# Performance work log

Hardware: AMD Instinct MI355X
Metric: run time of the kernel (lower is better)

## Reference

```python
import jax, jax.numpy as jnp
import numpy as np

GROUP_SIZE = 128
HIDDEN = 2048
INTER = 5632
TOKENS = 8192
_SHIFTS = jnp.arange(8, dtype=jnp.uint32) * 4  # 4-bit nibbles, 8 per int32


def _pack_rows(nib):
    # nib: [in, out] int values in [0,16); pack 8 consecutive rows into one int32
    r, c = nib.shape
    n = nib.reshape(r // 8, 8, c).astype(jnp.uint32)
    packed = jnp.sum(n << _SHIFTS[None, :, None], axis=1, dtype=jnp.uint32)
    return jax.lax.bitcast_convert_type(packed, jnp.int32)  # [in//8, out]


def _pack_cols(nib):
    # nib: [groups, out]; pack 8 consecutive cols into one int32
    g, o = nib.shape
    n = nib.reshape(g, o // 8, 8).astype(jnp.uint32)
    packed = jnp.sum(n << _SHIFTS[None, None, :], axis=-1, dtype=jnp.uint32)
    return jax.lax.bitcast_convert_type(packed, jnp.int32)  # [groups, out//8]


def _dequant(qweight, qzeros, scales, group_size=GROUP_SIZE):
    # GPTQ int4 dequant: w = (q - (z + 1)) * scale, per group of `group_size` input rows
    in_packed, out = qweight.shape
    in_dim = in_packed * 8
    groups = scales.shape[0]
    sh = jnp.arange(8, dtype=jnp.int32) * 4
    q = (qweight[:, None, :] >> sh[None, :, None]) & 0xF       # [in//8, 8, out]
    q = q.reshape(in_dim, out)
    z = (qzeros[:, :, None] >> sh[None, None, :]) & 0xF        # [groups, out//8, 8]
    z = z.reshape(groups, out)
    gidx = jnp.arange(in_dim) // group_size                    # [in]
    w = (q - (z[gidx] + 1)).astype(scales.dtype) * scales[gidx]
    return w  # [in, out]


def setup_inputs() -> dict:
    key = jax.random.key(0)
    ks = jax.random.split(key, 10)
    x = jax.random.normal(ks[0], (TOKENS, HIDDEN), dtype=jnp.float32)

    def make(kq, kz, ksc, in_dim, out_dim):
        qn = jax.random.randint(kq, (in_dim, out_dim), 0, 16, dtype=jnp.int32)
        zn = jax.random.randint(kz, (in_dim // GROUP_SIZE, out_dim), 0, 16, dtype=jnp.int32)
        sc = jax.random.uniform(ksc, (in_dim // GROUP_SIZE, out_dim), jnp.float32, 1e-3, 2e-2)
        return _pack_rows(qn), _pack_cols(zn), sc

    gq, gz, gs = make(ks[1], ks[2], ks[3], HIDDEN, INTER)
    uq, uz, us = make(ks[4], ks[5], ks[6], HIDDEN, INTER)
    dq, dz, ds = make(ks[7], ks[8], ks[9], INTER, HIDDEN)
    return {
        "x": x,
        "gate_qweight": gq, "gate_qzeros": gz, "gate_scales": gs,
        "up_qweight": uq, "up_qzeros": uz, "up_scales": us,
        "down_qweight": dq, "down_qzeros": dz, "down_scales": ds,
    }


def reference(x, gate_qweight, gate_qzeros, gate_scales,
              up_qweight, up_qzeros, up_scales,
              down_qweight, down_qzeros, down_scales):
    wg = _dequant(gate_qweight, gate_qzeros, gate_scales)  # [H, I]
    wu = _dequant(up_qweight, up_qzeros, up_scales)        # [H, I]
    wd = _dequant(down_qweight, down_qzeros, down_scales)  # [I, H]
    # fused_gate_up: silu(x @ Wg) * (x @ Wu)
    h = jax.nn.silu(x @ wg) * (x @ wu)                     # [T, I]
    return h @ wd                                          # [T, H]
```

## Files before the change

### kernel.cpp

```cpp
#include <hip/hip_runtime.h>
#include <stdint.h>

#define TOKENS 8192
#define HIDDEN 2048
#define INTER  5632

typedef _Float16 f16x8 __attribute__((ext_vector_type(8)));
typedef _Float16 f16x2 __attribute__((ext_vector_type(2)));
typedef float    f32x4 __attribute__((ext_vector_type(4)));
typedef unsigned int uint;

__device__ __forceinline__ void async_copy16(const void* g, void* l) {
  __builtin_amdgcn_global_load_lds(
      (const __attribute__((address_space(1))) uint*)g,
      (__attribute__((address_space(3))) uint*)l, 16, 0, 0);
}

union U8 { uint u[4]; f16x8 v; };
__device__ __forceinline__ f16x8 dq8(uint w, uint sd, uint zd) {
  const f16x2 s = __builtin_bit_cast(f16x2, sd);
  const f16x2 z = __builtin_bit_cast(f16x2, zd);
  U8 r;
  uint t0 = (w & 0x000F000Fu) | 0x64006400u;
  uint t1 = ((w >> 4) & 0x000F000Fu) | 0x64006400u;
  uint t2 = ((w >> 8) & 0x000F000Fu) | 0x64006400u;
  uint t3 = ((w >> 12) & 0x000F000Fu) | 0x64006400u;
  r.u[0] = __builtin_bit_cast(uint, (f16x2)((__builtin_bit_cast(f16x2, t0) - z) * s));
  r.u[1] = __builtin_bit_cast(uint, (f16x2)((__builtin_bit_cast(f16x2, t1) - z) * s));
  r.u[2] = __builtin_bit_cast(uint, (f16x2)((__builtin_bit_cast(f16x2, t2) - z) * s));
  r.u[3] = __builtin_bit_cast(uint, (f16x2)((__builtin_bit_cast(f16x2, t3) - z) * s));
  return r.v;
}

__device__ __forceinline__ uint dupf16(float x) {
  _Float16 h = (_Float16)x;
  unsigned short b = __builtin_bit_cast(unsigned short, h);
  return (uint)b * 0x00010001u;
}

__global__ void k_convert_x(const float* __restrict__ x, _Float16* __restrict__ xs) {
  const int kb = blockIdx.x;
  const int mt = blockIdx.y;
  const int m  = threadIdx.x;
  const float* src = x + (size_t)(mt * 128 + m) * HIDDEN + kb * 8;
  float4 f0 = *(const float4*)src;
  float4 f1 = *(const float4*)(src + 4);
  f16x8 v;
  v[0] = (_Float16)f0.x; v[1] = (_Float16)f1.x;
  v[2] = (_Float16)f0.y; v[3] = (_Float16)f1.y;
  v[4] = (_Float16)f0.z; v[5] = (_Float16)f1.z;
  v[6] = (_Float16)f0.w; v[7] = (_Float16)f1.w;
  *(f16x8*)(xs + ((size_t)(mt * 256 + kb) * 128 + m) * 8) = v;
}

__global__ void k_prep_szgu(const uint* __restrict__ gz, const float* __restrict__ gs,
                            const uint* __restrict__ uz, const float* __restrict__ us,
                            uint4* __restrict__ out) {
  const int n = blockIdx.x * 256 + threadIdx.x;
  const int g = blockIdx.y;
  const int sh = (n & 7) * 4;
  int zg = (int)((gz[(size_t)g * (INTER / 8) + (n >> 3)] >> sh) & 0xFu);
  int zu = (int)((uz[(size_t)g * (INTER / 8) + (n >> 3)] >> sh) & 0xFu);
  float sg = gs[(size_t)g * INTER + n];
  float su = us[(size_t)g * INTER + n];
  out[(size_t)g * INTER + n] =
      make_uint4(dupf16(sg), dupf16((float)(1025 + zg)),
                 dupf16(su), dupf16((float)(1025 + zu)));
}

__global__ void k_prep_szd(const uint* __restrict__ dz, const float* __restrict__ ds,
                           uint2* __restrict__ out) {
  const int n = blockIdx.x * 256 + threadIdx.x;
  const int g = blockIdx.y;
  const int sh = (n & 7) * 4;
  int z = (int)((dz[(size_t)g * (HIDDEN / 8) + (n >> 3)] >> sh) & 0xFu);
  float s = ds[(size_t)g * HIDDEN + n];
  out[(size_t)g * HIDDEN + n] = make_uint2(dupf16(s), dupf16((float)(1025 + z)));
}

__global__ __launch_bounds__(256, 2)
void k_gemm_gateup(const _Float16* __restrict__ xs,
                   const uint* __restrict__ gq,
                   const uint* __restrict__ uq,
                   const uint4* __restrict__ szgu,
                   _Float16* __restrict__ hs) {
  __shared__ char smem[16384 + 4096 + 4096 + 2048];
  _Float16* Al = (_Float16*)smem;
  char* Bgl = smem + 16384;
  char* Bul = smem + 20480;
  char* szl = smem + 24576;

  const int nt = blockIdx.x, mt = blockIdx.y;
  const int tid = threadIdx.x;
  const int wave = tid >> 6, lane = tid & 63;
  const int wm = wave >> 1, wn = wave & 1;
  const int row16 = lane >> 4, col = lane & 15;
  const int slot = wave * 4;

  const _Float16* gA = xs + (size_t)mt * 256 * 1024;

  const int brow = 2 * wave + (lane >> 5);
  const int bcolw = ((lane & 31) * 4) ^ ((brow & 1) << 4);
  const size_t bbase = (size_t)brow * INTER + nt * 128 + bcolw;

  int afo[4];
#pragma unroll
  for (int i = 0; i < 4; ++i)
    afo[i] = (row16 * 128 + wm * 64 + i * 16 + col) * 8;
  int bco[4];
  const int bswz = (row16 & 1) << 4;
#pragma unroll
  for (int ni = 0; ni < 4; ++ni)
    bco[ni] = (wn * 64 + ni * 16 + col) ^ bswz;

  const f32x4 zero = {0.f, 0.f, 0.f, 0.f};
  f32x4 accg[4][4], accu[4][4];
#pragma unroll
  for (int i = 0; i < 4; ++i)
#pragma unroll
    for (int j = 0; j < 4; ++j) { accg[i][j] = zero; accu[i][j] = zero; }

  uint2 szg[4], szu[4];

  for (int kit = 0; kit < HIDDEN / 64; ++kit) {
    __syncthreads();
#pragma unroll
    for (int q = 0; q < 4; ++q) {
      const int c2 = (slot + q) * 64 + lane;
      async_copy16(gA + (size_t)kit * 8192 + (size_t)c2 * 8,
                   (char*)Al + (slot + q) * 1024);
    }
    {
      const size_t go = (size_t)kit * 8 * INTER + bbase;
      async_copy16(gq + go, Bgl + wave * 1024);
      async_copy16(uq + go, Bul + wave * 1024);
    }
    if (((kit & 1) == 0) && wave < 2) {
      const int n = wave * 64 + lane;
      async_copy16(szgu + (size_t)(kit >> 1) * INTER + nt * 128 + n,
                   szl + wave * 1024);
    }
    __syncthreads();
    if ((kit & 1) == 0) {
#pragma unroll
      for (int ni = 0; ni < 4; ++ni) {
        const int n16 = (wn * 64 + ni * 16 + col) * 16;
        szg[ni] = *(const uint2*)(szl + n16);
        szu[ni] = *(const uint2*)(szl + n16 + 8);
      }
    }
#pragma unroll
    for (int ks = 0; ks < 2; ++ks) {
      const int kadd = ks * 4096;
      f16x8 af[4];
#pragma unroll
      for (int i = 0; i < 4; ++i)
        af[i] = *(const f16x8*)(Al + kadd + afo[i]);
      const int bks = (ks * 4 + row16) * 512;
      uint bgw[4], buw[4];
#pragma unroll
      for (int ni = 0; ni < 4; ++ni) {
        bgw[ni] = *(const uint*)(Bgl + bks + bco[ni] * 4);
        buw[ni] = *(const uint*)(Bul + bks + bco[ni] * 4);
      }
      f16x8 bgf[4], buf_[4];
#pragma unroll
      for (int ni = 0; ni < 4; ++ni) {
        bgf[ni] = dq8(bgw[ni], szg[ni].x, szg[ni].y);
        buf_[ni] = dq8(buw[ni], szu[ni].x, szu[ni].y);
      }
#pragma unroll
      for (int mi = 0; mi < 4; ++mi)
#pragma unroll
        for (int ni = 0; ni < 4; ++ni) {
          accg[mi][ni] = __builtin_amdgcn_mfma_f32_16x16x32_f16(af[mi], bgf[ni], accg[mi][ni], 0, 0, 0);
          accu[mi][ni] = __builtin_amdgcn_mfma_f32_16x16x32_f16(af[mi], buf_[ni], accu[mi][ni], 0, 0, 0);
        }
    }
  }
#pragma unroll
  for (int mi = 0; mi < 4; ++mi)
#pragma unroll
    for (int ni = 0; ni < 4; ++ni) {
      const int kg = nt * 128 + wn * 64 + ni * 16 + col;
      const int sub = kg & 7;
      const int pslot = ((sub & 3) << 1) | (sub >> 2);
      const size_t base = (size_t)(mt * (INTER / 8) + (kg >> 3)) * 1024 + pslot;
#pragma unroll
      for (int r = 0; r < 4; ++r) {
        float g = accg[mi][ni][r], u = accu[mi][ni][r];
        float h = g / (1.f + __expf(-g)) * u;
        const int ml = wm * 64 + mi * 16 + row16 * 4 + r;
        hs[base + (size_t)ml * 8] = (_Float16)h;
      }
    }
}

__global__ __launch_bounds__(256, 2)
void k_gemm_down(const _Float16* __restrict__ hs,
                 const uint* __restrict__ dq,
                 const uint2* __restrict__ szd,
                 float* __restrict__ out) {
  __shared__ char smem[16384 + 4096 + 1024];
  _Float16* Al = (_Float16*)smem;
  char* Bl  = smem + 16384;
  char* szl = smem + 20480;

  const int nt = blockIdx.x, mt = blockIdx.y;
  const int tid = threadIdx.x;
  const int wave = tid >> 6, lane = tid & 63;
  const int wm = wave >> 1, wn = wave & 1;
  const int row16 = lane >> 4, col = lane & 15;
  const int slot = wave * 4;

  const _Float16* gA = hs + (size_t)mt * (INTER / 8) * 1024;

  const int brow = 2 * wave + (lane >> 5);
  const int bcolw = ((lane & 31) * 4) ^ ((brow & 1) << 4);
  const size_t bbase = (size_t)brow * HIDDEN + nt * 128 + bcolw;

  int afo[4];
#pragma unroll
  for (int i = 0; i < 4; ++i)
    afo[i] = (row16 * 128 + wm * 64 + i * 16 + col) * 8;
  int bco[4];
  const int bswz = (row16 & 1) << 4;
#pragma unroll
  for (int ni = 0; ni < 4; ++ni)
    bco[ni] = (wn * 64 + ni * 16 + col) ^ bswz;

  const f32x4 zero = {0.f, 0.f, 0.f, 0.f};
  f32x4 acc[4][4];
#pragma unroll
  for (int i = 0; i < 4; ++i)
#pragma unroll
    for (int j = 0; j < 4; ++j) acc[i][j] = zero;

  uint2 sz[4];

  for (int kit = 0; kit < INTER / 64; ++kit) {
    __syncthreads();
#pragma unroll
    for (int q = 0; q < 4; ++q) {
      const int c2 = (slot + q) * 64 + lane;
      async_copy16(gA + (size_t)kit * 8192 + (size_t)c2 * 8,
                   (char*)Al + (slot + q) * 1024);
    }
    async_copy16(dq + (size_t)kit * 8 * HIDDEN + bbase, Bl + wave * 1024);
    if (((kit & 1) == 0) && wave == 0) {
      async_copy16(szd + (size_t)(kit >> 1) * HIDDEN + nt * 128 + lane * 2, szl);
    }
    __syncthreads();
    if ((kit & 1) == 0) {
#pragma unroll
      for (int ni = 0; ni < 4; ++ni) {
        const int n8 = (wn * 64 + ni * 16 + col) * 8;
        sz[ni] = *(const uint2*)(szl + n8);
      }
    }
#pragma unroll
    for (int ks = 0; ks < 2; ++ks) {
      const int kadd = ks * 4096;
      f16x8 af[4];
#pragma unroll
      for (int i = 0; i < 4; ++i)
        af[i] = *(const f16x8*)(Al + kadd + afo[i]);
      const int bks = (ks * 4 + row16) * 512;
      uint bw[4];
#pragma unroll
      for (int ni = 0; ni < 4; ++ni)
        bw[ni] = *(const uint*)(Bl + bks + bco[ni] * 4);
      f16x8 bf[4];
#pragma unroll
      for (int ni = 0; ni < 4; ++ni)
        bf[ni] = dq8(bw[ni], sz[ni].x, sz[ni].y);
#pragma unroll
      for (int mi = 0; mi < 4; ++mi)
#pragma unroll
        for (int ni = 0; ni < 4; ++ni)
          acc[mi][ni] = __builtin_amdgcn_mfma_f32_16x16x32_f16(af[mi], bf[ni], acc[mi][ni], 0, 0, 0);
    }
  }
#pragma unroll
  for (int mi = 0; mi < 4; ++mi)
#pragma unroll
    for (int ni = 0; ni < 4; ++ni) {
      const int n = nt * 128 + wn * 64 + ni * 16 + col;
#pragma unroll
      for (int r = 0; r < 4; ++r) {
        const int m = mt * 128 + wm * 64 + mi * 16 + row16 * 4 + r;
        out[(size_t)m * HIDDEN + n] = acc[mi][ni][r];
      }
    }
}

extern "C" void kernel_launch(void* const* d_in, const int* in_sizes, int n_in,
                              void* d_out, int out_size, void* d_ws, size_t ws_size,
                              hipStream_t stream) {
  (void)in_sizes; (void)n_in; (void)out_size; (void)ws_size;
  const float* x  = (const float*)d_in[0];
  const uint*  gq = (const uint*)d_in[1];
  const uint*  gz = (const uint*)d_in[2];
  const float* gs = (const float*)d_in[3];
  const uint*  uq = (const uint*)d_in[4];
  const uint*  uz = (const uint*)d_in[5];
  const float* us = (const float*)d_in[6];
  const uint*  dq = (const uint*)d_in[7];
  const uint*  dz = (const uint*)d_in[8];
  const float* ds = (const float*)d_in[9];
  float* out = (float*)d_out;

  char* ws = (char*)d_ws;
  _Float16* xs  = (_Float16*)ws;
  _Float16* hs  = (_Float16*)(ws + (size_t)TOKENS * HIDDEN * 2);
  uint4* szgu = (uint4*)(ws + (size_t)TOKENS * HIDDEN * 2 + (size_t)TOKENS * INTER * 2);
  uint2* szd  = (uint2*)((char*)szgu + (size_t)16 * INTER * 16);

  k_convert_x<<<dim3(HIDDEN / 8, TOKENS / 128), 128, 0, stream>>>(x, xs);
  k_prep_szgu<<<dim3(INTER / 256, HIDDEN / 128), 256, 0, stream>>>(gz, gs, uz, us, szgu);
  k_prep_szd<<<dim3(HIDDEN / 256, INTER / 128), 256, 0, stream>>>(dz, ds, szd);
  k_gemm_gateup<<<dim3(INTER / 128, TOKENS / 128), 256, 0, stream>>>(xs, gq, uq, szgu, hs);
  k_gemm_down<<<dim3(HIDDEN / 128, TOKENS / 128), 256, 0, stream>>>(hs, dq, szd, out);
}
```

Before: 776.7 us.

## Switch both GEMMs from 16x16x32 to 32x32x16 MFMA with new wave tiling

Measured after the change: 792.8 us. 1.02x slower.

```diff
diff --git a/kernel.cpp b/kernel.cpp
--- a/kernel.cpp
+++ b/kernel.cpp
@@ -5,9 +5,9 @@
 #define HIDDEN 2048
 #define INTER  5632
 
-typedef _Float16 f16x8 __attribute__((ext_vector_type(8)));
-typedef _Float16 f16x2 __attribute__((ext_vector_type(2)));
-typedef float    f32x4 __attribute__((ext_vector_type(4)));
+typedef _Float16 f16x8  __attribute__((ext_vector_type(8)));
+typedef _Float16 f16x2  __attribute__((ext_vector_type(2)));
+typedef float    f32x16 __attribute__((ext_vector_type(16)));
 typedef unsigned int uint;
 
 __device__ __forceinline__ void async_copy16(const void* g, void* l) {
@@ -20,11 +20,11 @@
 __device__ __forceinline__ f16x8 dq8(uint w, uint sd, uint zd) {
   const f16x2 s = __builtin_bit_cast(f16x2, sd);
   const f16x2 z = __builtin_bit_cast(f16x2, zd);
+  uint t0 = ( w        & 0x000F000Fu) | 0x64006400u;
+  uint t1 = ((w >> 4)  & 0x000F000Fu) | 0x64006400u;
+  uint t2 = ((w >> 8)  & 0x000F000Fu) | 0x64006400u;
+  uint t3 = ((w >> 12) & 0x000F000Fu) | 0x64006400u;
   U8 r;
-  uint t0 = (w & 0x000F000Fu) | 0x64006400u;
-  uint t1 = ((w >> 4) & 0x000F000Fu) | 0x64006400u;
-  uint t2 = ((w >> 8) & 0x000F000Fu) | 0x64006400u;
-  uint t3 = ((w >> 12) & 0x000F000Fu) | 0x64006400u;
   r.u[0] = __builtin_bit_cast(uint, (f16x2)((__builtin_bit_cast(f16x2, t0) - z) * s));
   r.u[1] = __builtin_bit_cast(uint, (f16x2)((__builtin_bit_cast(f16x2, t1) - z) * s));
   r.u[2] = __builtin_bit_cast(uint, (f16x2)((__builtin_bit_cast(f16x2, t2) - z) * s));
@@ -34,8 +34,8 @@
 
 __device__ __forceinline__ uint dupf16(float x) {
   _Float16 h = (_Float16)x;
-  unsigned short b = __builtin_bit_cast(unsigned short, h);
-  return (uint)b * 0x00010001u;
+  unsigned short bb = __builtin_bit_cast(unsigned short, h);
+  return (uint)bb * 0x00010001u;
 }
 
 __global__ void k_convert_x(const float* __restrict__ x, _Float16* __restrict__ xs) {
@@ -93,42 +93,33 @@
   const int nt = blockIdx.x, mt = blockIdx.y;
   const int tid = threadIdx.x;
   const int wave = tid >> 6, lane = tid & 63;
-  const int wm = wave >> 1, wn = wave & 1;
-  const int row16 = lane >> 4, col = lane & 15;
-  const int slot = wave * 4;
+  const int lane31 = lane & 31, row_h = lane >> 5;
 
   const _Float16* gA = xs + (size_t)mt * 256 * 1024;
 
-  const int brow = 2 * wave + (lane >> 5);
-  const int bcolw = ((lane & 31) * 4) ^ ((brow & 1) << 4);
+  const int brow = 2 * wave + row_h;
+  const int bcolw = (lane31 * 4) ^ ((brow & 1) << 4);
   const size_t bbase = (size_t)brow * INTER + nt * 128 + bcolw;
 
-  int afo[4];
-#pragma unroll
-  for (int i = 0; i < 4; ++i)
-    afo[i] = (row16 * 128 + wm * 64 + i * 16 + col) * 8;
-  int bco[4];
-  const int bswz = (row16 & 1) << 4;
-#pragma unroll
-  for (int ni = 0; ni < 4; ++ni)
-    bco[ni] = (wn * 64 + ni * 16 + col) ^ bswz;
-
-  const f32x4 zero = {0.f, 0.f, 0.f, 0.f};
-  f32x4 accg[4][4], accu[4][4];
-#pragma unroll
-  for (int i = 0; i < 4; ++i)
-#pragma unroll
-    for (int j = 0; j < 4; ++j) { accg[i][j] = zero; accu[i][j] = zero; }
-
-  uint2 szg[4], szu[4];
+  const int n_loc = 32 * wave + lane31;
+  const int bread = row_h * 512 + ((n_loc ^ (row_h << 4)) * 4);
+  const int aread = row_h * 2048 + lane31 * 16;
+
+  f32x16 accg[4], accu[4];
+#pragma unroll
+  for (int i = 0; i < 4; ++i) {
+    accg[i] = (f32x16)0.f; accu[i] = (f32x16)0.f;
+  }
+
+  uint sg = 0, zg = 0, su = 0, zu = 0;
 
   for (int kit = 0; kit < HIDDEN / 64; ++kit) {
     __syncthreads();
 #pragma unroll
     for (int q = 0; q < 4; ++q) {
-      const int c2 = (slot + q) * 64 + lane;
+      const int c2 = (wave * 4 + q) * 64 + lane;
       async_copy16(gA + (size_t)kit * 8192 + (size_t)c2 * 8,
-                   (char*)Al + (slot + q) * 1024);
+                   (char*)Al + (wave * 4 + q) * 1024);
     }
     {
       const size_t go = (size_t)kit * 8 * INTER + bbase;
@@ -136,64 +127,46 @@
       async_copy16(uq + go, Bul + wave * 1024);
     }
     if (((kit & 1) == 0) && wave < 2) {
-      const int n = wave * 64 + lane;
-      async_copy16(szgu + (size_t)(kit >> 1) * INTER + nt * 128 + n,
+      async_copy16(szgu + (size_t)(kit >> 1) * INTER + nt * 128 + wave * 64 + lane,
                    szl + wave * 1024);
     }
     __syncthreads();
     if ((kit & 1) == 0) {
-#pragma unroll
-      for (int ni = 0; ni < 4; ++ni) {
-        const int n16 = (wn * 64 + ni * 16 + col) * 16;
-        szg[ni] = *(const uint2*)(szl + n16);
-        szu[ni] = *(const uint2*)(szl + n16 + 8);
+      uint4 v = *(const uint4*)(szl + n_loc * 16);
+      sg = v.x; zg = v.y; su = v.z; zu = v.w;
+    }
+#pragma unroll
+    for (int kt = 0; kt < 4; ++kt) {
+      f16x8 af[4];
+#pragma unroll
+      for (int mi = 0; mi < 4; ++mi)
+        af[mi] = *(const f16x8*)((char*)Al + kt * 4096 + aread + mi * 512);
+      const uint wgw = *(const uint*)(Bgl + kt * 1024 + bread);
+      const uint wuw = *(const uint*)(Bul + kt * 1024 + bread);
+      const f16x8 bgf = dq8(wgw, sg, zg);
+      const f16x8 buf_ = dq8(wuw, su, zu);
+#pragma unroll
+      for (int mi = 0; mi < 4; ++mi) {
+        accg[mi] = __builtin_amdgcn_mfma_f32_32x32x16_f16(af[mi], bgf, accg[mi], 0, 0, 0);
+        accu[mi] = __builtin_amdgcn_mfma_f32_32x32x16_f16(af[mi], buf_, accu[mi], 0, 0, 0);
       }
     }
-#pragma unroll
-    for (int ks = 0; ks < 2; ++ks) {
-      const int kadd = ks * 4096;
-      f16x8 af[4];
-#pragma unroll
-      for (int i = 0; i < 4; ++i)
-        af[i] = *(const f16x8*)(Al + kadd + afo[i]);
-      const int bks = (ks * 4 + row16) * 512;
-      uint bgw[4], buw[4];
-#pragma unroll
-      for (int ni = 0; ni < 4; ++ni) {
-        bgw[ni] = *(const uint*)(Bgl + bks + bco[ni] * 4);
-        buw[ni] = *(const uint*)(Bul + bks + bco[ni] * 4);
-      }
-      f16x8 bgf[4], buf_[4];
-#pragma unroll
-      for (int ni = 0; ni < 4; ++ni) {
-        bgf[ni] = dq8(bgw[ni], szg[ni].x, szg[ni].y);
-        buf_[ni] = dq8(buw[ni], szu[ni].x, szu[ni].y);
-      }
-#pragma unroll
-      for (int mi = 0; mi < 4; ++mi)
-#pragma unroll
-        for (int ni = 0; ni < 4; ++ni) {
-          accg[mi][ni] = __builtin_amdgcn_mfma_f32_16x16x32_f16(af[mi], bgf[ni], accg[mi][ni], 0, 0, 0);
-          accu[mi][ni] = __builtin_amdgcn_mfma_f32_16x16x32_f16(af[mi], buf_[ni], accu[mi][ni], 0, 0, 0);
-        }
-    }
-  }
-#pragma unroll
-  for (int mi = 0; mi < 4; ++mi)
-#pragma unroll
-    for (int ni = 0; ni < 4; ++ni) {
-      const int kg = nt * 128 + wn * 64 + ni * 16 + col;
-      const int sub = kg & 7;
-      const int pslot = ((sub & 3) << 1) | (sub >> 2);
-      const size_t base = (size_t)(mt * (INTER / 8) + (kg >> 3)) * 1024 + pslot;
-#pragma unroll
-      for (int r = 0; r < 4; ++r) {
-        float g = accg[mi][ni][r], u = accu[mi][ni][r];
-        float h = g / (1.f + __expf(-g)) * u;
-        const int ml = wm * 64 + mi * 16 + row16 * 4 + r;
-        hs[base + (size_t)ml * 8] = (_Float16)h;
-      }
-    }
+  }
+  const int kg = nt * 128 + n_loc;
+  const int sub = kg & 7;
+  const int pslot = ((sub & 3) << 1) | (sub >> 2);
+  const size_t base = (size_t)(mt * (INTER / 8) + (kg >> 3)) * 1024 + pslot;
+#pragma unroll
+  for (int mi = 0; mi < 4; ++mi) {
+#pragma unroll
+    for (int r = 0; r < 16; ++r) {
+      float g = accg[mi][r], u = accu[mi][r];
+      float h = g / (1.f + __expf(-g)) * u;
+      const int row = (r & 3) + 8 * (r >> 2) + 4 * row_h;
+      const int ml = 32 * mi + row;
+      hs[base + (size_t)ml * 8] = (_Float16)h;
+    }
+  }
 }
 
 __global__ __launch_bounds__(256, 2)
@@ -209,42 +182,38 @@
   const int nt = blockIdx.x, mt = blockIdx.y;
   const int tid = threadIdx.x;
   const int wave = tid >> 6, lane = tid & 63;
+  const int lane31 = lane & 31, row_h = lane >> 5;
   const int wm = wave >> 1, wn = wave & 1;
-  const int row16 = lane >> 4, col = lane & 15;
-  const int slot = wave * 4;
 
   const _Float16* gA = hs + (size_t)mt * (INTER / 8) * 1024;
 
-  const int brow = 2 * wave + (lane >> 5);
-  const int bcolw = ((lane & 31) * 4) ^ ((brow & 1) << 4);
+  const int brow = 2 * wave + row_h;
+  const int bcolw = (lane31 * 4) ^ ((brow & 1) << 4);
   const size_t bbase = (size_t)brow * HIDDEN + nt * 128 + bcolw;
 
-  int afo[4];
-#pragma unroll
-  for (int i = 0; i < 4; ++i)
-    afo[i] = (row16 * 128 + wm * 64 + i * 16 + col) * 8;
-  int bco[4];
-  const int bswz = (row16 & 1) << 4;
-#pragma unroll
-  for (int ni = 0; ni < 4; ++ni)
-    bco[ni] = (wn * 64 + ni * 16 + col) ^ bswz;
-
-  const f32x4 zero = {0.f, 0.f, 0.f, 0.f};
-  f32x4 acc[4][4];
-#pragma unroll
-  for (int i = 0; i < 4; ++i)
-#pragma unroll
-    for (int j = 0; j < 4; ++j) acc[i][j] = zero;
-
-  uint2 sz[4];
+  int nl[2], bread[2], aread[2];
+#pragma unroll
+  for (int i = 0; i < 2; ++i) {
+    nl[i] = 64 * wn + 32 * i + lane31;
+    bread[i] = row_h * 512 + ((nl[i] ^ (row_h << 4)) * 4);
+    aread[i] = row_h * 2048 + (64 * wm + 32 * i + lane31) * 16;
+  }
+
+  f32x16 acc[2][2];
+#pragma unroll
+  for (int i = 0; i < 2; ++i)
+#pragma unroll
+    for (int j = 0; j < 2; ++j) acc[i][j] = (f32x16)0.f;
+
+  uint s0 = 0, z0 = 0, s1 = 0, z1 = 0;
 
   for (int kit = 0; kit < INTER / 64; ++kit) {
     __syncthreads();
 #pragma unroll
     for (int q = 0; q < 4; ++q) {
-      const int c2 = (slot + q) * 64 + lane;
+      const int c2 = (wave * 4 + q) * 64 + lane;
       async_copy16(gA + (size_t)kit * 8192 + (size_t)c2 * 8,
-                   (char*)Al + (slot + q) * 1024);
+                   (char*)Al + (wave * 4 + q) * 1024);
     }
     async_copy16(dq + (size_t)kit * 8 * HIDDEN + bbase, Bl + wave * 1024);
     if (((kit & 1) == 0) && wave == 0) {
@@ -252,43 +221,36 @@
     }
     __syncthreads();
     if ((kit & 1) == 0) {
-#pragma unroll
-      for (int ni = 0; ni < 4; ++ni) {
-        const int n8 = (wn * 64 + ni * 16 + col) * 8;
-        sz[ni] = *(const uint2*)(szl + n8);
+      uint2 v0 = *(const uint2*)(szl + nl[0] * 8);
+      uint2 v1 = *(const uint2*)(szl + nl[1] * 8);
+      s0 = v0.x; z0 = v0.y; s1 = v1.x; z1 = v1.y;
+    }
+#pragma unroll
+    for (int kt = 0; kt < 4; ++kt) {
+      f16x8 af[2];
+#pragma unroll
+      for (int mi = 0; mi < 2; ++mi)
+        af[mi] = *(const f16x8*)((char*)Al + kt * 4096 + aread[mi]);
+      const uint w0 = *(const uint*)(Bl + kt * 1024 + bread[0]);
+      const uint w1 = *(const uint*)(Bl + kt * 1024 + bread[1]);
+      const f16x8 bf0 = dq8(w0, s0, z0);
+      const f16x8 bf1 = dq8(w1, s1, z1);
+#pragma unroll
+      for (int mi = 0; mi < 2; ++mi) {
+        acc[mi][0] = __builtin_amdgcn_mfma_f32_32x32x16_f16(af[mi], bf0, acc[mi][0], 0, 0, 0);
+        acc[mi][1] = __builtin_amdgcn_mfma_f32_32x32x16_f16(af[mi], bf1, acc[mi][1], 0, 0, 0);
       }
     }
-#pragma unroll
-    for (int ks = 0; ks < 2; ++ks) {
-      const int kadd = ks * 4096;
-      f16x8 af[4];
-#pragma unroll
-      for (int i = 0; i < 4; ++i)
-        af[i] = *(const f16x8*)(Al + kadd + afo[i]);
-      const int bks = (ks * 4 + row16) * 512;
-      uint bw[4];
-#pragma unroll
-      for (int ni = 0; ni < 4; ++ni)
-        bw[ni] = *(const uint*)(Bl + bks + bco[ni] * 4);
-      f16x8 bf[4];
-#pragma unroll
-      for (int ni = 0; ni < 4; ++ni)
-        bf[ni] = dq8(bw[ni], sz[ni].x, sz[ni].y);
-#pragma unroll
-      for (int mi = 0; mi < 4; ++mi)
-#pragma unroll
-        for (int ni = 0; ni < 4; ++ni)
-          acc[mi][ni] = __builtin_amdgcn_mfma_f32_16x16x32_f16(af[mi], bf[ni], acc[mi][ni], 0, 0, 0);
-    }
-  }
-#pragma unroll
-  for (int mi = 0; mi < 4; ++mi)
-#pragma unroll
-    for (int ni = 0; ni < 4; ++ni) {
-      const int n = nt * 128 + wn * 64 + ni * 16 + col;
-#pragma unroll
-      for (int r = 0; r < 4; ++r) {
-        const int m = mt * 128 + wm * 64 + mi * 16 + row16 * 4 + r;
+  }
+#pragma unroll
+  for (int mi = 0; mi < 2; ++mi)
+#pragma unroll
+    for (int ni = 0; ni < 2; ++ni) {
+      const int n = nt * 128 + nl[ni];
+#pragma unroll
+      for (int r = 0; r < 16; ++r) {
+        const int row = (r & 3) + 8 * (r >> 2) + 4 * row_h;
+        const int m = mt * 128 + 64 * wm + 32 * mi + row;
         out[(size_t)m * HIDDEN + n] = acc[mi][ni][r];
       }
     }
```
